# Performance work log

Measured on AMD Instinct MI355X. Metric: run time of the kernel, lower is better.

Reference implementation:

```python
import jax, jax.numpy as jnp
from jax import lax
import numpy as np

B, T, D, H = 256, 512, 64, 256

def setup_inputs() -> dict:
    key = jax.random.key(0)
    ks = jax.random.split(key, 15)
    s = lambda fan_in: 1.0 / np.sqrt(fan_in)
    def lin(k, out_d, in_d):
        k1, k2 = jax.random.split(k)
        return (jax.random.uniform(k1, (out_d, in_d), jnp.float32, -s(in_d), s(in_d)),
                jax.random.uniform(k2, (out_d,), jnp.float32, -s(in_d), s(in_d)))
    W1_w, W1_b = lin(ks[0], H, D)
    U1_w, U1_b = lin(ks[1], H, H)
    W2_w, W2_b = lin(ks[2], H, H)
    U2_w, U2_b = lin(ks[3], H, H)
    o1_w, o1_b = lin(ks[4], D, H)
    o2_w, o2_b = lin(ks[5], D, H)
    g_w, g_b = lin(ks[6], H, 2 * H)
    x = jax.random.normal(ks[7], (B, T, D), jnp.float32)
    return {"x": x, "W1_w": W1_w, "W1_b": W1_b, "U1_w": U1_w, "U1_b": U1_b,
            "W2_w": W2_w, "W2_b": W2_b, "U2_w": U2_w, "U2_b": U2_b,
            "o1_w": o1_w, "o1_b": o1_b, "o2_w": o2_w, "o2_b": o2_b,
            "g_w": g_w, "g_b": g_b}


def reference(x, W1_w, W1_b, U1_w, U1_b, W2_w, W2_b, U2_w, U2_b,
              o1_w, o1_b, o2_w, o2_b, g_w, g_b):
    Bb, Tt, Dd = x.shape
    Hh = U1_w.shape[0]
    h1_0 = jnp.zeros((Bb, Hh), x.dtype)
    h2_0 = jnp.zeros((Bb, Hh), x.dtype)
    u_0 = jnp.ones((Bb, Hh), x.dtype)  # initial gate = 1 (broadcast of ones(1,1))

    def step(carry, xt):
        h1, h2, u = carry
        h1 = jnp.tanh(xt @ W1_w.T + W1_b + h1 @ U1_w.T + U1_b)
        h2_new = jnp.tanh(h1 @ W2_w.T + W2_b + h2 @ U2_w.T + U2_b)
        h2 = u * h2_new + (1.0 - u) * h2
        out = h1 @ o1_w.T + o1_b + h2 @ o2_w.T + o2_b  # (B, D)
        u = jax.nn.sigmoid(jnp.concatenate([h1, h2], axis=1) @ g_w.T + g_b)
        return (h1, h2, u), out

    _, outs = lax.scan(step, (h1_0, h2_0, u_0), jnp.swapaxes(x, 0, 1))  # (T, B, D)
    return jnp.swapaxes(outs, 0, 1)  # (B, T, D)
```

## Files before the change

kernel.cpp:

```cpp
#include <hip/hip_runtime.h>

typedef unsigned short u16;
using bf8   = __attribute__((ext_vector_type(8))) short;
using bf4   = __attribute__((ext_vector_type(4))) short;
using f32x4 = __attribute__((ext_vector_type(4))) float;

#define B_ 256
#define T_ 512
#define D_ 64
#define H_ 256
#define Tc_ 64
#define NC_ (T_ / Tc_)
#define GEMMB_ 192

#define MFMA(a, b, c) __builtin_amdgcn_mfma_f32_16x16x32_bf16(a, b, c, 0, 0, 0)

static __device__ inline u16 f2b(float f) {
    unsigned int u = __float_as_uint(f);
    unsigned int r = (u + 0x7fffu + ((u >> 16) & 1u)) >> 16;
    return (u16)r;
}
static __device__ inline float fast_tanh(float x) {
    float e = __expf(2.f * x);
    return 1.f - 2.f / (e + 1.f);
}
static __device__ inline float fast_sigmoid(float x) {
    return 1.f / (1.f + __expf(-x));
}
static __device__ inline void lds_barrier() {
    asm volatile("s_waitcnt lgkmcnt(0)" ::: "memory");
    __builtin_amdgcn_s_barrier();
    asm volatile("" ::: "memory");
}

__global__ __launch_bounds__(256) void k_conv(
    const float* __restrict__ W1w, const float* __restrict__ U1w,
    const float* __restrict__ W2w, const float* __restrict__ U2w,
    const float* __restrict__ o1w, const float* __restrict__ o2w,
    const float* __restrict__ gw,
    u16* W1bf, u16* U1bf, u16* W2bf, u16* U2bf,
    u16* o1bf, u16* o2bf, u16* gbf)
{
    const int a = blockIdx.y;
    const float* src; u16* dst; int n;
    switch (a) {
        case 0: src = W1w; dst = W1bf; n = 16384;  break;
        case 1: src = U1w; dst = U1bf; n = 65536;  break;
        case 2: src = W2w; dst = W2bf; n = 65536;  break;
        case 3: src = U2w; dst = U2bf; n = 65536;  break;
        case 4: src = o1w; dst = o1bf; n = 16384;  break;
        case 5: src = o2w; dst = o2bf; n = 16384;  break;
        default: src = gw; dst = gbf;  n = 131072; break;
    }
    const int i = (blockIdx.x * 256 + threadIdx.x) * 4;
    if (i < n) {
        f32x4 v = *(const f32x4*)(src + i);
        bf4 o;
        o[0] = (short)f2b(v[0]); o[1] = (short)f2b(v[1]);
        o[2] = (short)f2b(v[2]); o[3] = (short)f2b(v[3]);
        *(bf4*)(dst + i) = o;
    }
}

__device__ void h1_role(
    const float* __restrict__ x, const u16* __restrict__ W1,
    const u16* __restrict__ U1, const float* __restrict__ W1b,
    const float* __restrict__ U1b, u16* __restrict__ H1,
    u16* __restrict__ h1state, int c, u16 (*buf)[16][H_ + 8])
{
    const int g = blockIdx.x;
    const int tid = threadIdx.x;
    const int w = tid >> 6, lane = tid & 63;
    const int col = lane & 15, quad = lane >> 4;
    const int t0 = c * Tc_;

    bf8 u1f[2][8], w1f[2][2];
    float bias[2];
#pragma unroll
    for (int i = 0; i < 2; ++i) {
        const int n = (w * 2 + i) * 16 + col;
#pragma unroll
        for (int kt = 0; kt < 8; ++kt)
            u1f[i][kt] = *(const bf8*)(U1 + (size_t)n * H_ + kt * 32 + quad * 8);
#pragma unroll
        for (int kt = 0; kt < 2; ++kt)
            w1f[i][kt] = *(const bf8*)(W1 + (size_t)n * D_ + kt * 32 + quad * 8);
        bias[i] = W1b[n] + U1b[n];
    }

    if (c == 0) {
        for (int idx = tid; idx < 16 * (H_ + 8); idx += 512)
            ((u16*)buf[0])[idx] = 0;
    } else {
        const int m = tid >> 5, hb = (tid & 31) * 8;
#pragma unroll
        for (int j = 0; j < 8; ++j)
            buf[0][m][hb + j] = h1state[(size_t)(g * 16 + m) * H_ + hb + j];
    }
    __syncthreads();

    const float* xrow = x + (size_t)(g * 16 + col) * T_ * D_ + quad * 8;
    f32x4 xa[4];
    {
        const float* xp = xrow + (size_t)t0 * D_;
        xa[0] = *(const f32x4*)xp;        xa[1] = *(const f32x4*)(xp + 4);
        xa[2] = *(const f32x4*)(xp + 32); xa[3] = *(const f32x4*)(xp + 36);
    }

    int p = 0;
    for (int tt = 0; tt < Tc_; ++tt) {
        const int tn = t0 + (tt + 1 < Tc_ ? tt + 1 : tt);
        f32x4 xan[4];
        {
            const float* xp = xrow + (size_t)tn * D_;
            xan[0] = *(const f32x4*)xp;        xan[1] = *(const f32x4*)(xp + 4);
            xan[2] = *(const f32x4*)(xp + 32); xan[3] = *(const f32x4*)(xp + 36);
        }
        bf8 haf[8];
#pragma unroll
        for (int kt = 0; kt < 8; ++kt)
            haf[kt] = *(const bf8*)&buf[p][col][kt * 32 + quad * 8];

        bf8 xaf[2];
#pragma unroll
        for (int kt = 0; kt < 2; ++kt) {
            bf8 v;
#pragma unroll
            for (int j = 0; j < 4; ++j) {
                v[j]     = (short)f2b(xa[kt * 2][j]);
                v[j + 4] = (short)f2b(xa[kt * 2 + 1][j]);
            }
            xaf[kt] = v;
        }

        f32x4 acc[2];
#pragma unroll
        for (int i = 0; i < 2; ++i) {
            acc[i][0] = bias[i]; acc[i][1] = bias[i];
            acc[i][2] = bias[i]; acc[i][3] = bias[i];
        }
#pragma unroll
        for (int kt = 0; kt < 8; ++kt)
#pragma unroll
            for (int i = 0; i < 2; ++i)
                acc[i] = MFMA(haf[kt], u1f[i][kt], acc[i]);
#pragma unroll
        for (int kt = 0; kt < 2; ++kt)
#pragma unroll
            for (int i = 0; i < 2; ++i)
                acc[i] = MFMA(xaf[kt], w1f[i][kt], acc[i]);

#pragma unroll
        for (int i = 0; i < 2; ++i) {
            const int n = (w * 2 + i) * 16 + col;
#pragma unroll
            for (int r = 0; r < 4; ++r)
                buf[p ^ 1][quad * 4 + r][n] = f2b(fast_tanh(acc[i][r]));
        }
        lds_barrier();
        {
            const int m = tid >> 5, hb = (tid & 31) * 8;
            bf8 v0 = *(const bf8*)&buf[p ^ 1][m][hb];
            *(bf8*)(H1 + ((size_t)tt * 256 + g * 16 + m) * H_ + hb) = v0;
        }
        xa[0] = xan[0]; xa[1] = xan[1]; xa[2] = xan[2]; xa[3] = xan[3];
        p ^= 1;
    }
    {
        const int m = tid >> 5, hb = (tid & 31) * 8;
#pragma unroll
        for (int j = 0; j < 8; ++j)
            h1state[(size_t)(g * 16 + m) * H_ + hb + j] = buf[p][m][hb + j];
    }
}

__device__ void h2_role(
    const u16* __restrict__ U2, const u16* __restrict__ gw,
    const float* __restrict__ W2c, const float* __restrict__ G1c,
    u16* __restrict__ H2, float* __restrict__ h2state,
    float* __restrict__ ustate, int ch, u16 (*buf)[16][H_ + 8])
{
    const int g = blockIdx.x - 16;
    const int tid = threadIdx.x;
    const int w = tid >> 6, lane = tid & 63;
    const int col = lane & 15, quad = lane >> 4;

    bf8 u2f[2][8], g2f[2][8];
#pragma unroll
    for (int i = 0; i < 2; ++i) {
        const int n = (w * 2 + i) * 16 + col;
#pragma unroll
        for (int kt = 0; kt < 8; ++kt) {
            u2f[i][kt] = *(const bf8*)(U2 + (size_t)n * H_ + kt * 32 + quad * 8);
            g2f[i][kt] = *(const bf8*)(gw + (size_t)n * (2 * H_) + H_ + kt * 32 + quad * 8);
        }
    }

    f32x4 h2p[2], up[2];
    if (ch == 0) {
#pragma unroll
        for (int i = 0; i < 2; ++i) {
            h2p[i][0]=0.f; h2p[i][1]=0.f; h2p[i][2]=0.f; h2p[i][3]=0.f;
            up[i][0]=1.f;  up[i][1]=1.f;  up[i][2]=1.f;  up[i][3]=1.f;
        }
    } else {
#pragma unroll
        for (int i = 0; i < 2; ++i) {
            size_t idx = (((size_t)g * 16 + (w * 2 + i)) * 64 + lane) * 4;
            h2p[i] = *(const f32x4*)(h2state + idx);
            up[i]  = *(const f32x4*)(ustate + idx);
        }
    }

#pragma unroll
    for (int i = 0; i < 2; ++i) {
        const int n = (w * 2 + i) * 16 + col;
#pragma unroll
        for (int r = 0; r < 4; ++r) buf[0][quad * 4 + r][n] = f2b(h2p[i][r]);
    }
    __syncthreads();
    bf8 h2af[8];
#pragma unroll
    for (int kt = 0; kt < 8; ++kt)
        h2af[kt] = *(const bf8*)&buf[0][col][kt * 32 + quad * 8];

    f32x4 w2cr[2];
#pragma unroll
    for (int i = 0; i < 2; ++i)
        w2cr[i] = *(const f32x4*)(W2c +
            ((((size_t)g * Tc_ + 0) * 16 + (w * 2 + i)) * 64 + lane) * 4);

    int p = 0;
    for (int tt = 0; tt < Tc_; ++tt) {
        const int ttn = (tt + 1 < Tc_) ? tt + 1 : tt;
        f32x4 w2cn[2], g1cc[2];
#pragma unroll
        for (int i = 0; i < 2; ++i) {
            w2cn[i] = *(const f32x4*)(W2c +
                ((((size_t)g * Tc_ + ttn) * 16 + (w * 2 + i)) * 64 + lane) * 4);
            g1cc[i] = *(const f32x4*)(G1c +
                ((((size_t)g * Tc_ + tt) * 16 + (w * 2 + i)) * 64 + lane) * 4);
        }

        f32x4 acc1[2];
#pragma unroll
        for (int i = 0; i < 2; ++i) acc1[i] = w2cr[i];
#pragma unroll
        for (int kt = 0; kt < 8; ++kt)
#pragma unroll
            for (int i = 0; i < 2; ++i)
                acc1[i] = MFMA(h2af[kt], u2f[i][kt], acc1[i]);

#pragma unroll
        for (int i = 0; i < 2; ++i)
#pragma unroll
            for (int r = 0; r < 4; ++r) {
                float h2n = fast_tanh(acc1[i][r]);
                h2p[i][r] = up[i][r] * h2n + (1.f - up[i][r]) * h2p[i][r];
            }
#pragma unroll
        for (int i = 0; i < 2; ++i) {
            const int n = (w * 2 + i) * 16 + col;
#pragma unroll
            for (int r = 0; r < 4; ++r) buf[p ^ 1][quad * 4 + r][n] = f2b(h2p[i][r]);
        }
        lds_barrier();
#pragma unroll
        for (int kt = 0; kt < 8; ++kt)
            h2af[kt] = *(const bf8*)&buf[p ^ 1][col][kt * 32 + quad * 8];
        {
            const int m = tid >> 5, hb = (tid & 31) * 8;
            bf8 v0 = *(const bf8*)&buf[p ^ 1][m][hb];
            *(bf8*)(H2 + ((size_t)tt * 256 + g * 16 + m) * H_ + hb) = v0;
        }

        f32x4 accg[2];
#pragma unroll
        for (int i = 0; i < 2; ++i) accg[i] = g1cc[i];
#pragma unroll
        for (int kt = 0; kt < 8; ++kt)
#pragma unroll
            for (int i = 0; i < 2; ++i)
                accg[i] = MFMA(h2af[kt], g2f[i][kt], accg[i]);
#pragma unroll
        for (int i = 0; i < 2; ++i)
#pragma unroll
            for (int r = 0; r < 4; ++r) up[i][r] = fast_sigmoid(accg[i][r]);

#pragma unroll
        for (int i = 0; i < 2; ++i) w2cr[i] = w2cn[i];
        p ^= 1;
    }
#pragma unroll
    for (int i = 0; i < 2; ++i) {
        size_t idx = (((size_t)g * 16 + (w * 2 + i)) * 64 + lane) * 4;
        *(f32x4*)(h2state + idx) = h2p[i];
        *(f32x4*)(ustate + idx)  = up[i];
    }
}

__global__ __launch_bounds__(512)
__attribute__((amdgpu_waves_per_eu(2, 2))) void k_pipe(
    const float* __restrict__ x, const u16* __restrict__ W1,
    const u16* __restrict__ U1, const float* __restrict__ W1b,
    const float* __restrict__ U1b, u16* __restrict__ H1w,
    u16* __restrict__ h1state,
    const u16* __restrict__ U2, const u16* __restrict__ gwgt,
    const float* __restrict__ W2cr, const float* __restrict__ G1cr,
    u16* __restrict__ H2w, float* __restrict__ h2state,
    float* __restrict__ ustate,
    const u16* __restrict__ H1r, const u16* __restrict__ W2,
    const u16* __restrict__ o1w, const u16* __restrict__ o2w,
    const float* __restrict__ W2b, const float* __restrict__ U2b,
    const float* __restrict__ gbias, const float* __restrict__ o1b,
    const float* __restrict__ o2b,
    float* __restrict__ W2cw, float* __restrict__ G1cw, float* __restrict__ O1cw,
    const u16* __restrict__ H2r, const float* __restrict__ O1r,
    float* __restrict__ out, int c)
{
    __shared__ __align__(16) u16 buf[2][16][H_ + 8];
    if (blockIdx.x < 16) {
        if (c < NC_)
            h1_role(x, W1, U1, W1b, U1b, H1w, h1state, c, buf);
    } else if (blockIdx.x < 32) {
        if (c >= 2 && c <= NC_ + 1)
            h2_role(U2, gwgt, W2cr, G1cr, H2w, h2state, ustate, c - 2, buf);
    } else {
        const int gbk = blockIdx.x - 32;
        const int tid = threadIdx.x;
        const int w = tid >> 6, lane = tid & 63;
        const int col = lane & 15, quad = lane >> 4;
        const int Wv = gbk * 8 + w;
        const int ny = Wv % 10;
        const int j  = Wv / 10;
        if (j >= 153) return;
        const bool act = (ny < 9) ? (c >= 1 && c <= NC_)
                                  : (c >= 3 && c <= NC_ + 2);
        if (!act) return;

        bf8 bfv[4][8];
        float bias[4];
#pragma unroll
        for (int i = 0; i < 4; ++i) {
            const int n = ny * 64 + i * 16 + col;
            const u16* bp; float bs;
            if (n < 256)      { bp = W2   + (size_t)n * H_;             bs = W2b[n] + U2b[n]; }
            else if (n < 512) { bp = gwgt + (size_t)(n - 256) * (2*H_); bs = gbias[n - 256]; }
            else if (n < 576) { bp = o1w  + (size_t)(n - 512) * H_;     bs = o1b[n-512] + o2b[n-512]; }
            else              { bp = o2w  + (size_t)(n - 576) * H_;     bs = 0.f; }
            bias[i] = bs;
#pragma unroll
            for (int kt = 0; kt < 8; ++kt)
                bfv[i][kt] = *(const bf8*)(bp + kt * 32 + quad * 8);
        }

        const u16* Ar = (ny < 9) ? H1r : H2r;
        float* Cb = W2cw; int ntb = 0;
        if (ny < 4)       { Cb = W2cw; ntb = ny * 4; }
        else if (ny < 8)  { Cb = G1cw; ntb = ny * 4 - 16; }
        else if (ny == 8) { Cb = O1cw; ntb = 0; }
        const int tb = (c - 3) * Tc_;

        for (int mt = j; mt < 1024; mt += 153) {
            const int mrow = mt * 16;
            f32x4 acc[4];
#pragma unroll
            for (int i = 0; i < 4; ++i) {
                acc[i][0] = bias[i]; acc[i][1] = bias[i];
                acc[i][2] = bias[i]; acc[i][3] = bias[i];
            }
#pragma unroll
            for (int kt = 0; kt < 8; ++kt) {
                bf8 af = *(const bf8*)(Ar + (size_t)(mrow + col) * H_ + kt * 32 + quad * 8);
#pragma unroll
                for (int i = 0; i < 4; ++i)
                    acc[i] = MFMA(af, bfv[i][kt], acc[i]);
            }
            const int tt = mrow >> 8, gg = (mrow & 255) >> 4;
            if (ny < 8) {
#pragma unroll
                for (int i = 0; i < 4; ++i) {
                    size_t idx = ((((size_t)gg * Tc_ + tt) * 16 + (ntb + i)) * 64 + lane) * 4;
                    *(f32x4*)(Cb + idx) = acc[i];
                }
            } else if (ny == 8) {
#pragma unroll
                for (int i = 0; i < 4; ++i) {
                    size_t idx = ((((size_t)gg * Tc_ + tt) * 4 + i) * 64 + lane) * 4;
                    *(f32x4*)(Cb + idx) = acc[i];
                }
            } else {
#pragma unroll
                for (int i = 0; i < 4; ++i) {
                    f32x4 o1v = *(const f32x4*)(O1r +
                        ((((size_t)gg * Tc_ + tt) * 4 + i) * 64 + lane) * 4);
#pragma unroll
                    for (int r = 0; r < 4; ++r)
                        out[((size_t)(gg * 16 + quad * 4 + r) * T_ + (tb + tt)) * D_ +
                            i * 16 + col] = acc[i][r] + o1v[r];
                }
            }
        }
    }
}

extern "C" void kernel_launch(void* const* d_in, const int* in_sizes, int n_in,
                              void* d_out, int out_size, void* d_ws, size_t ws_size,
                              hipStream_t stream)
{
    const float* x   = (const float*)d_in[0];
    const float* W1w = (const float*)d_in[1];
    const float* W1b = (const float*)d_in[2];
    const float* U1w = (const float*)d_in[3];
    const float* U1b = (const float*)d_in[4];
    const float* W2w = (const float*)d_in[5];
    const float* W2b = (const float*)d_in[6];
    const float* U2w = (const float*)d_in[7];
    const float* U2b = (const float*)d_in[8];
    const float* o1w = (const float*)d_in[9];
    const float* o1b = (const float*)d_in[10];
    const float* o2w = (const float*)d_in[11];
    const float* o2b = (const float*)d_in[12];
    const float* gw  = (const float*)d_in[13];
    const float* gb  = (const float*)d_in[14];
    float* out = (float*)d_out;
    (void)in_sizes; (void)n_in; (void)out_size; (void)ws_size;

    char* p = (char*)d_ws;
    u16* W1bf = (u16*)p; p += 16384 * 2;
    u16* U1bf = (u16*)p; p += 65536 * 2;
    u16* W2bf = (u16*)p; p += 65536 * 2;
    u16* U2bf = (u16*)p; p += 65536 * 2;
    u16* o1bf = (u16*)p; p += 16384 * 2;
    u16* o2bf = (u16*)p; p += 16384 * 2;
    u16* gbf  = (u16*)p; p += 131072 * 2;
    u16* H1[2]; u16* H2[2]; float* W2c[2]; float* G1c[2]; float* O1c[3];
    for (int pa = 0; pa < 2; ++pa) {
        H1[pa]  = (u16*)p;   p += (size_t)Tc_ * 131072;
        H2[pa]  = (u16*)p;   p += (size_t)Tc_ * 131072;
        W2c[pa] = (float*)p; p += (size_t)Tc_ * 262144;
        G1c[pa] = (float*)p; p += (size_t)Tc_ * 262144;
    }
    for (int pa = 0; pa < 3; ++pa) {
        O1c[pa] = (float*)p; p += (size_t)Tc_ * 65536;
    }
    u16* h1s   = (u16*)p;  p += 131072;
    float* h2s = (float*)p; p += 262144;
    float* us  = (float*)p;

    k_conv<<<dim3(128, 7), 256, 0, stream>>>(W1w, U1w, W2w, U2w, o1w, o2w, gw,
                                             W1bf, U1bf, W2bf, U2bf, o1bf, o2bf, gbf);

    for (int c = 0; c <= NC_ + 2; ++c) {
        const int pw  = c & 1;
        const int pg  = (c + 1) & 1;
        const int ph  = c & 1;
        const int s_w = ((c - 1) % 3 + 3) % 3;
        const int s_r = ((c - 3) % 3 + 3) % 3;
        k_pipe<<<32 + GEMMB_, 512, 0, stream>>>(
            x, W1bf, U1bf, W1b, U1b, H1[pw], h1s,
            U2bf, gbf, W2c[ph], G1c[ph], H2[pw], h2s, us,
            H1[pg], W2bf, o1bf, o2bf, W2b, U2b, gb, o1b, o2b,
            W2c[pg], G1c[pg], O1c[s_w],
            H2[pg], O1c[s_r], out, c);
    }
}
```

Measured before the change: 1.204 ms.

## Double block size to 1024 threads, one 16-column tile per wave

After: 1.604 ms. 1.33x slower.

```diff
diff --git a/kernel.cpp b/kernel.cpp
--- a/kernel.cpp
+++ b/kernel.cpp
@@ -11,7 +11,7 @@
 #define H_ 256
 #define Tc_ 64
 #define NC_ (T_ / Tc_)
-#define GEMMB_ 192
+#define GEMMB_ 190
 
 #define MFMA(a, b, c) __builtin_amdgcn_mfma_f32_16x16x32_bf16(a, b, c, 0, 0, 0)
 
@@ -73,29 +73,24 @@
     const int w = tid >> 6, lane = tid & 63;
     const int col = lane & 15, quad = lane >> 4;
     const int t0 = c * Tc_;
-
-    bf8 u1f[2][8], w1f[2][2];
-    float bias[2];
-#pragma unroll
-    for (int i = 0; i < 2; ++i) {
-        const int n = (w * 2 + i) * 16 + col;
-#pragma unroll
-        for (int kt = 0; kt < 8; ++kt)
-            u1f[i][kt] = *(const bf8*)(U1 + (size_t)n * H_ + kt * 32 + quad * 8);
-#pragma unroll
-        for (int kt = 0; kt < 2; ++kt)
-            w1f[i][kt] = *(const bf8*)(W1 + (size_t)n * D_ + kt * 32 + quad * 8);
-        bias[i] = W1b[n] + U1b[n];
-    }
+    const int n = w * 16 + col;
+
+    bf8 u1f[8], w1f[2];
+#pragma unroll
+    for (int kt = 0; kt < 8; ++kt)
+        u1f[kt] = *(const bf8*)(U1 + (size_t)n * H_ + kt * 32 + quad * 8);
+#pragma unroll
+    for (int kt = 0; kt < 2; ++kt)
+        w1f[kt] = *(const bf8*)(W1 + (size_t)n * D_ + kt * 32 + quad * 8);
+    const float bias = W1b[n] + U1b[n];
 
     if (c == 0) {
-        for (int idx = tid; idx < 16 * (H_ + 8); idx += 512)
+        for (int idx = tid; idx < 16 * (H_ + 8); idx += 1024)
             ((u16*)buf[0])[idx] = 0;
     } else {
-        const int m = tid >> 5, hb = (tid & 31) * 8;
-#pragma unroll
-        for (int j = 0; j < 8; ++j)
-            buf[0][m][hb + j] = h1state[(size_t)(g * 16 + m) * H_ + hb + j];
+        const int m = tid >> 6, hb = (tid & 63) * 4;
+        *(bf4*)&buf[0][m][hb] =
+            *(const bf4*)(h1state + (size_t)(g * 16 + m) * H_ + hb);
     }
     __syncthreads();
 
@@ -133,44 +128,31 @@
             xaf[kt] = v;
         }
 
-        f32x4 acc[2];
-#pragma unroll
-        for (int i = 0; i < 2; ++i) {
-            acc[i][0] = bias[i]; acc[i][1] = bias[i];
-            acc[i][2] = bias[i]; acc[i][3] = bias[i];
-        }
+        f32x4 acc;
+        acc[0] = bias; acc[1] = bias; acc[2] = bias; acc[3] = bias;
 #pragma unroll
         for (int kt = 0; kt < 8; ++kt)
-#pragma unroll
-            for (int i = 0; i < 2; ++i)
-                acc[i] = MFMA(haf[kt], u1f[i][kt], acc[i]);
+            acc = MFMA(haf[kt], u1f[kt], acc);
 #pragma unroll
         for (int kt = 0; kt < 2; ++kt)
-#pragma unroll
-            for (int i = 0; i < 2; ++i)
-                acc[i] = MFMA(xaf[kt], w1f[i][kt], acc[i]);
-
-#pragma unroll
-        for (int i = 0; i < 2; ++i) {
-            const int n = (w * 2 + i) * 16 + col;
-#pragma unroll
-            for (int r = 0; r < 4; ++r)
-                buf[p ^ 1][quad * 4 + r][n] = f2b(fast_tanh(acc[i][r]));
-        }
+            acc = MFMA(xaf[kt], w1f[kt], acc);
+
+#pragma unroll
+        for (int r = 0; r < 4; ++r)
+            buf[p ^ 1][quad * 4 + r][n] = f2b(fast_tanh(acc[r]));
         lds_barrier();
         {
-            const int m = tid >> 5, hb = (tid & 31) * 8;
-            bf8 v0 = *(const bf8*)&buf[p ^ 1][m][hb];
-            *(bf8*)(H1 + ((size_t)tt * 256 + g * 16 + m) * H_ + hb) = v0;
+            const int m = tid >> 6, hb = (tid & 63) * 4;
+            bf4 v0 = *(const bf4*)&buf[p ^ 1][m][hb];
+            *(bf4*)(H1 + ((size_t)tt * 256 + g * 16 + m) * H_ + hb) = v0;
         }
         xa[0] = xan[0]; xa[1] = xan[1]; xa[2] = xan[2]; xa[3] = xan[3];
         p ^= 1;
     }
     {
-        const int m = tid >> 5, hb = (tid & 31) * 8;
-#pragma unroll
-        for (int j = 0; j < 8; ++j)
-            h1state[(size_t)(g * 16 + m) * H_ + hb + j] = buf[p][m][hb + j];
+        const int m = tid >> 6, hb = (tid & 63) * 4;
+        *(bf4*)(h1state + (size_t)(g * 16 + m) * H_ + hb) =
+            *(const bf4*)&buf[p][m][hb];
     }
 }
 
@@ -184,123 +166,84 @@
     const int tid = threadIdx.x;
     const int w = tid >> 6, lane = tid & 63;
     const int col = lane & 15, quad = lane >> 4;
-
-    bf8 u2f[2][8], g2f[2][8];
-#pragma unroll
-    for (int i = 0; i < 2; ++i) {
-        const int n = (w * 2 + i) * 16 + col;
-#pragma unroll
-        for (int kt = 0; kt < 8; ++kt) {
-            u2f[i][kt] = *(const bf8*)(U2 + (size_t)n * H_ + kt * 32 + quad * 8);
-            g2f[i][kt] = *(const bf8*)(gw + (size_t)n * (2 * H_) + H_ + kt * 32 + quad * 8);
-        }
-    }
-
-    f32x4 h2p[2], up[2];
+    const int n = w * 16 + col;
+
+    bf8 u2f[8], g2f[8];
+#pragma unroll
+    for (int kt = 0; kt < 8; ++kt) {
+        u2f[kt] = *(const bf8*)(U2 + (size_t)n * H_ + kt * 32 + quad * 8);
+        g2f[kt] = *(const bf8*)(gw + (size_t)n * (2 * H_) + H_ + kt * 32 + quad * 8);
+    }
+
+    f32x4 h2p, up;
     if (ch == 0) {
-#pragma unroll
-        for (int i = 0; i < 2; ++i) {
-            h2p[i][0]=0.f; h2p[i][1]=0.f; h2p[i][2]=0.f; h2p[i][3]=0.f;
-            up[i][0]=1.f;  up[i][1]=1.f;  up[i][2]=1.f;  up[i][3]=1.f;
-        }
+        h2p[0]=0.f; h2p[1]=0.f; h2p[2]=0.f; h2p[3]=0.f;
+        up[0]=1.f;  up[1]=1.f;  up[2]=1.f;  up[3]=1.f;
     } else {
-#pragma unroll
-        for (int i = 0; i < 2; ++i) {
-            size_t idx = (((size_t)g * 16 + (w * 2 + i)) * 64 + lane) * 4;
-            h2p[i] = *(const f32x4*)(h2state + idx);
-            up[i]  = *(const f32x4*)(ustate + idx);
-        }
-    }
-
-#pragma unroll
-    for (int i = 0; i < 2; ++i) {
-        const int n = (w * 2 + i) * 16 + col;
-#pragma unroll
-        for (int r = 0; r < 4; ++r) buf[0][quad * 4 + r][n] = f2b(h2p[i][r]);
-    }
+        size_t idx = (((size_t)g * 16 + w) * 64 + lane) * 4;
+        h2p = *(const f32x4*)(h2state + idx);
+        up  = *(const f32x4*)(ustate + idx);
+    }
+
+#pragma unroll
+    for (int r = 0; r < 4; ++r) buf[0][quad * 4 + r][n] = f2b(h2p[r]);
     __syncthreads();
     bf8 h2af[8];
 #pragma unroll
     for (int kt = 0; kt < 8; ++kt)
         h2af[kt] = *(const bf8*)&buf[0][col][kt * 32 + quad * 8];
 
-    f32x4 w2cr[2];
-#pragma unroll
-    for (int i = 0; i < 2; ++i)
-        w2cr[i] = *(const f32x4*)(W2c +
-            ((((size_t)g * Tc_ + 0) * 16 + (w * 2 + i)) * 64 + lane) * 4);
+    f32x4 w2cr = *(const f32x4*)(W2c +
+        ((((size_t)g * Tc_ + 0) * 16 + w) * 64 + lane) * 4);
 
     int p = 0;
     for (int tt = 0; tt < Tc_; ++tt) {
         const int ttn = (tt + 1 < Tc_) ? tt + 1 : tt;
-        f32x4 w2cn[2], g1cc[2];
-#pragma unroll
-        for (int i = 0; i < 2; ++i) {
-            w2cn[i] = *(const f32x4*)(W2c +
-                ((((size_t)g * Tc_ + ttn) * 16 + (w * 2 + i)) * 64 + lane) * 4);
-            g1cc[i] = *(const f32x4*)(G1c +
-                ((((size_t)g * Tc_ + tt) * 16 + (w * 2 + i)) * 64 + lane) * 4);
-        }
-
-        f32x4 acc1[2];
-#pragma unroll
-        for (int i = 0; i < 2; ++i) acc1[i] = w2cr[i];
+        f32x4 w2cn = *(const f32x4*)(W2c +
+            ((((size_t)g * Tc_ + ttn) * 16 + w) * 64 + lane) * 4);
+        f32x4 g1cc = *(const f32x4*)(G1c +
+            ((((size_t)g * Tc_ + tt) * 16 + w) * 64 + lane) * 4);
+
+        f32x4 acc1 = w2cr;
 #pragma unroll
         for (int kt = 0; kt < 8; ++kt)
-#pragma unroll
-            for (int i = 0; i < 2; ++i)
-                acc1[i] = MFMA(h2af[kt], u2f[i][kt], acc1[i]);
-
-#pragma unroll
-        for (int i = 0; i < 2; ++i)
-#pragma unroll
-            for (int r = 0; r < 4; ++r) {
-                float h2n = fast_tanh(acc1[i][r]);
-                h2p[i][r] = up[i][r] * h2n + (1.f - up[i][r]) * h2p[i][r];
-            }
-#pragma unroll
-        for (int i = 0; i < 2; ++i) {
-            const int n = (w * 2 + i) * 16 + col;
-#pragma unroll
-            for (int r = 0; r < 4; ++r) buf[p ^ 1][quad * 4 + r][n] = f2b(h2p[i][r]);
-        }
+            acc1 = MFMA(h2af[kt], u2f[kt], acc1);
+
+#pragma unroll
+        for (int r = 0; r < 4; ++r) {
+            float h2n = fast_tanh(acc1[r]);
+            h2p[r] = up[r] * h2n + (1.f - up[r]) * h2p[r];
+        }
+#pragma unroll
+        for (int r = 0; r < 4; ++r) buf[p ^ 1][quad * 4 + r][n] = f2b(h2p[r]);
         lds_barrier();
 #pragma unroll
         for (int kt = 0; kt < 8; ++kt)
             h2af[kt] = *(const bf8*)&buf[p ^ 1][col][kt * 32 + quad * 8];
         {
-            const int m = tid >> 5, hb = (tid & 31) * 8;
-            bf8 v0 = *(const bf8*)&buf[p ^ 1][m][hb];
-            *(bf8*)(H2 + ((size_t)tt * 256 + g * 16 + m) * H_ + hb) = v0;
-        }
-
-        f32x4 accg[2];
-#pragma unroll
-        for (int i = 0; i < 2; ++i) accg[i] = g1cc[i];
+            const int m = tid >> 6, hb = (tid & 63) * 4;
+            bf4 v0 = *(const bf4*)&buf[p ^ 1][m][hb];
+            *(bf4*)(H2 + ((size_t)tt * 256 + g * 16 + m) * H_ + hb) = v0;
+        }
+
+        f32x4 accg = g1cc;
 #pragma unroll
         for (int kt = 0; kt < 8; ++kt)
-#pragma unroll
-            for (int i = 0; i < 2; ++i)
-                accg[i] = MFMA(h2af[kt], g2f[i][kt], accg[i]);
-#pragma unroll
-        for (int i = 0; i < 2; ++i)
-#pragma unroll
-            for (int r = 0; r < 4; ++r) up[i][r] = fast_sigmoid(accg[i][r]);
-
-#pragma unroll
-        for (int i = 0; i < 2; ++i) w2cr[i] = w2cn[i];
+            accg = MFMA(h2af[kt], g2f[kt], accg);
+#pragma unroll
+        for (int r = 0; r < 4; ++r) up[r] = fast_sigmoid(accg[r]);
+
+        w2cr = w2cn;
         p ^= 1;
     }
-#pragma unroll
-    for (int i = 0; i < 2; ++i) {
-        size_t idx = (((size_t)g * 16 + (w * 2 + i)) * 64 + lane) * 4;
-        *(f32x4*)(h2state + idx) = h2p[i];
-        *(f32x4*)(ustate + idx)  = up[i];
-    }
-}
-
-__global__ __launch_bounds__(512)
-__attribute__((amdgpu_waves_per_eu(2, 2))) void k_pipe(
+    {
+        size_t idx = (((size_t)g * 16 + w) * 64 + lane) * 4;
+        *(f32x4*)(h2state + idx) = h2p;
+        *(f32x4*)(ustate + idx)  = up;
+    }
+}
+
+__global__ __launch_bounds__(1024) void k_pipe(
     const float* __restrict__ x, const u16* __restrict__ W1,
     const u16* __restrict__ U1, const float* __restrict__ W1b,
     const float* __restrict__ U1b, u16* __restrict__ H1w,
@@ -330,74 +273,77 @@
         const int tid = threadIdx.x;
         const int w = tid >> 6, lane = tid & 63;
         const int col = lane & 15, quad = lane >> 4;
-        const int Wv = gbk * 8 + w;
-        const int ny = Wv % 10;
-        const int j  = Wv / 10;
-        if (j >= 153) return;
-        const bool act = (ny < 9) ? (c >= 1 && c <= NC_)
-                                  : (c >= 3 && c <= NC_ + 2);
+        const int Wv = gbk * 16 + w;
+        const int unit = Wv % 20;
+        const int j = Wv / 20;
+        const bool act = (unit < 18) ? (c >= 1 && c <= NC_)
+                                     : (c >= 3 && c <= NC_ + 2);
         if (!act) return;
 
-        bf8 bfv[4][8];
-        float bias[4];
-#pragma unroll
-        for (int i = 0; i < 4; ++i) {
-            const int n = ny * 64 + i * 16 + col;
+        bf8 bfv[2][8];
+        float bias[2];
+#pragma unroll
+        for (int i = 0; i < 2; ++i) {
             const u16* bp; float bs;
-            if (n < 256)      { bp = W2   + (size_t)n * H_;             bs = W2b[n] + U2b[n]; }
-            else if (n < 512) { bp = gwgt + (size_t)(n - 256) * (2*H_); bs = gbias[n - 256]; }
-            else if (n < 576) { bp = o1w  + (size_t)(n - 512) * H_;     bs = o1b[n-512] + o2b[n-512]; }
-            else              { bp = o2w  + (size_t)(n - 576) * H_;     bs = 0.f; }
+            if (unit < 18) {
+                const int n = unit * 32 + i * 16 + col;
+                if (n < 256)      { bp = W2   + (size_t)n * H_;             bs = W2b[n] + U2b[n]; }
+                else if (n < 512) { bp = gwgt + (size_t)(n - 256) * (2*H_); bs = gbias[n - 256]; }
+                else              { bp = o1w  + (size_t)(n - 512) * H_;     bs = o1b[n-512] + o2b[n-512]; }
+            } else {
+                const int n = (unit - 18) * 32 + i * 16 + col;
+                bp = o2w + (size_t)n * H_; bs = 0.f;
+            }
             bias[i] = bs;
 #pragma unroll
             for (int kt = 0; kt < 8; ++kt)
                 bfv[i][kt] = *(const bf8*)(bp + kt * 32 + quad * 8);
         }
 
-        const u16* Ar = (ny < 9) ? H1r : H2r;
-        float* Cb = W2cw; int ntb = 0;
-        if (ny < 4)       { Cb = W2cw; ntb = ny * 4; }
-        else if (ny < 8)  { Cb = G1cw; ntb = ny * 4 - 16; }
-        else if (ny == 8) { Cb = O1cw; ntb = 0; }
+        const u16* Ar = (unit < 18) ? H1r : H2r;
         const int tb = (c - 3) * Tc_;
 
-        for (int mt = j; mt < 1024; mt += 153) {
+        for (int mt = j; mt < 1024; mt += 152) {
             const int mrow = mt * 16;
-            f32x4 acc[4];
-#pragma unroll
-            for (int i = 0; i < 4; ++i) {
+            f32x4 acc[2];
+#pragma unroll
+            for (int i = 0; i < 2; ++i) {
                 acc[i][0] = bias[i]; acc[i][1] = bias[i];
                 acc[i][2] = bias[i]; acc[i][3] = bias[i];
             }
 #pragma unroll
             for (int kt = 0; kt < 8; ++kt) {
                 bf8 af = *(const bf8*)(Ar + (size_t)(mrow + col) * H_ + kt * 32 + quad * 8);
-#pragma unroll
-                for (int i = 0; i < 4; ++i)
-                    acc[i] = MFMA(af, bfv[i][kt], acc[i]);
+                acc[0] = MFMA(af, bfv[0][kt], acc[0]);
+                acc[1] = MFMA(af, bfv[1][kt], acc[1]);
             }
-            const int tt = mrow >> 8, gg = (mrow & 255) >> 4;
-            if (ny < 8) {
-#pragma unroll
-                for (int i = 0; i < 4; ++i) {
-                    size_t idx = ((((size_t)gg * Tc_ + tt) * 16 + (ntb + i)) * 64 + lane) * 4;
+            const int tt = mt >> 4, gg = mt & 15;
+            if (unit < 16) {
+#pragma unroll
+                for (int i = 0; i < 2; ++i) {
+                    const int nt = unit * 2 + i;
+                    float* Cb = (nt < 16) ? W2cw : G1cw;
+                    const int nn = nt & 15;
+                    size_t idx = ((((size_t)gg * Tc_ + tt) * 16 + nn) * 64 + lane) * 4;
                     *(f32x4*)(Cb + idx) = acc[i];
                 }
-            } else if (ny == 8) {
-#pragma unroll
-                for (int i = 0; i < 4; ++i) {
-                    size_t idx = ((((size_t)gg * Tc_ + tt) * 4 + i) * 64 + lane) * 4;
-                    *(f32x4*)(Cb + idx) = acc[i];
+            } else if (unit < 18) {
+#pragma unroll
+                for (int i = 0; i < 2; ++i) {
+                    const int ot = (unit - 16) * 2 + i;
+                    size_t idx = ((((size_t)gg * Tc_ + tt) * 4 + ot) * 64 + lane) * 4;
+                    *(f32x4*)(O1cw + idx) = acc[i];
                 }
             } else {
 #pragma unroll
-                for (int i = 0; i < 4; ++i) {
+                for (int i = 0; i < 2; ++i) {
+                    const int ot = (unit - 18) * 2 + i;
                     f32x4 o1v = *(const f32x4*)(O1r +
-                        ((((size_t)gg * Tc_ + tt) * 4 + i) * 64 + lane) * 4);
+                        ((((size_t)gg * Tc_ + tt) * 4 + ot) * 64 + lane) * 4);
 #pragma unroll
                     for (int r = 0; r < 4; ++r)
                         out[((size_t)(gg * 16 + quad * 4 + r) * T_ + (tb + tt)) * D_ +
-                            i * 16 + col] = acc[i][r] + o1v[r];
+                            ot * 16 + col] = acc[i][r] + o1v[r];
                 }
             }
         }
@@ -457,7 +403,7 @@
         const int ph  = c & 1;
         const int s_w = ((c - 1) % 3 + 3) % 3;
         const int s_r = ((c - 3) % 3 + 3) % 3;
-        k_pipe<<<32 + GEMMB_, 512, 0, stream>>>(
+        k_pipe<<<32 + GEMMB_, 1024, 0, stream>>>(
             x, W1bf, U1bf, W1b, U1b, H1[pw], h1s,
             U2bf, gbf, W2c[ph], G1c[ph], H2[pw], h2s, us,
             H1[pg], W2bf, o1bf, o2bf, W2b, U2b, gb, o1b, o2b,
```

## Stage recurrent U1/U2 weights in LDS instead of registers

Applied to the files above, without the earlier changes.

New measurement: 1.359 ms. +12.9%, slower.

```diff
diff --git a/kernel.cpp b/kernel.cpp
--- a/kernel.cpp
+++ b/kernel.cpp
@@ -31,6 +31,15 @@
     asm volatile("s_waitcnt lgkmcnt(0)" ::: "memory");
     __builtin_amdgcn_s_barrier();
     asm volatile("" ::: "memory");
+}
+
+static __device__ inline void stage_weights(
+    u16* __restrict__ wlds, const u16* __restrict__ W, int tid)
+{
+    for (int idx = tid; idx < 8192; idx += 512) {
+        const int n = idx & 255, kc = idx >> 8;
+        *(bf8*)&wlds[(size_t)idx * 8] = *(const bf8*)(W + (size_t)n * 256 + kc * 8);
+    }
 }
 
 __global__ __launch_bounds__(256) void k_conv(
@@ -66,22 +75,24 @@
     const float* __restrict__ x, const u16* __restrict__ W1,
     const u16* __restrict__ U1, const float* __restrict__ W1b,
     const float* __restrict__ U1b, u16* __restrict__ H1,
-    u16* __restrict__ h1state, int c, u16 (*buf)[16][H_ + 8])
+    u16* __restrict__ h1state, int c, u16 (*buf)[16][H_ + 8],
+    u16* __restrict__ wlds)
 {
     const int g = blockIdx.x;
     const int tid = threadIdx.x;
     const int w = tid >> 6, lane = tid & 63;
     const int col = lane & 15, quad = lane >> 4;
     const int t0 = c * Tc_;
-
-    bf8 u1f[2][8], w1f[2][2];
+    const int n0 = (w * 2) * 16 + col;
+    const int n1 = (w * 2 + 1) * 16 + col;
+
+    stage_weights(wlds, U1, tid);
+
+    bf8 w1f[2][2];
     float bias[2];
 #pragma unroll
     for (int i = 0; i < 2; ++i) {
         const int n = (w * 2 + i) * 16 + col;
-#pragma unroll
-        for (int kt = 0; kt < 8; ++kt)
-            u1f[i][kt] = *(const bf8*)(U1 + (size_t)n * H_ + kt * 32 + quad * 8);
 #pragma unroll
         for (int kt = 0; kt < 2; ++kt)
             w1f[i][kt] = *(const bf8*)(W1 + (size_t)n * D_ + kt * 32 + quad * 8);
@@ -116,10 +127,21 @@
             xan[0] = *(const f32x4*)xp;        xan[1] = *(const f32x4*)(xp + 4);
             xan[2] = *(const f32x4*)(xp + 32); xan[3] = *(const f32x4*)(xp + 36);
         }
-        bf8 haf[8];
-#pragma unroll
-        for (int kt = 0; kt < 8; ++kt)
-            haf[kt] = *(const bf8*)&buf[p][col][kt * 32 + quad * 8];
+
+        f32x4 acc[2];
+#pragma unroll
+        for (int i = 0; i < 2; ++i) {
+            acc[i][0] = bias[i]; acc[i][1] = bias[i];
+            acc[i][2] = bias[i]; acc[i][3] = bias[i];
+        }
+#pragma unroll
+        for (int kt = 0; kt < 8; ++kt) {
+            bf8 hf = *(const bf8*)&buf[p][col][kt * 32 + quad * 8];
+            bf8 u0 = *(const bf8*)&wlds[(size_t)(((kt * 4 + quad) * 256) + n0) * 8];
+            bf8 u1v = *(const bf8*)&wlds[(size_t)(((kt * 4 + quad) * 256) + n1) * 8];
+            acc[0] = MFMA(hf, u0, acc[0]);
+            acc[1] = MFMA(hf, u1v, acc[1]);
+        }
 
         bf8 xaf[2];
 #pragma unroll
@@ -132,18 +154,6 @@
             }
             xaf[kt] = v;
         }
-
-        f32x4 acc[2];
-#pragma unroll
-        for (int i = 0; i < 2; ++i) {
-            acc[i][0] = bias[i]; acc[i][1] = bias[i];
-            acc[i][2] = bias[i]; acc[i][3] = bias[i];
-        }
-#pragma unroll
-        for (int kt = 0; kt < 8; ++kt)
-#pragma unroll
-            for (int i = 0; i < 2; ++i)
-                acc[i] = MFMA(haf[kt], u1f[i][kt], acc[i]);
 #pragma unroll
         for (int kt = 0; kt < 2; ++kt)
 #pragma unroll
@@ -178,22 +188,25 @@
     const u16* __restrict__ U2, const u16* __restrict__ gw,
     const float* __restrict__ W2c, const float* __restrict__ G1c,
     u16* __restrict__ H2, float* __restrict__ h2state,
-    float* __restrict__ ustate, int ch, u16 (*buf)[16][H_ + 8])
+    float* __restrict__ ustate, int ch, u16 (*buf)[16][H_ + 8],
+    u16* __restrict__ wlds)
 {
     const int g = blockIdx.x - 16;
     const int tid = threadIdx.x;
     const int w = tid >> 6, lane = tid & 63;
     const int col = lane & 15, quad = lane >> 4;
-
-    bf8 u2f[2][8], g2f[2][8];
+    const int n0 = (w * 2) * 16 + col;
+    const int n1 = (w * 2 + 1) * 16 + col;
+
+    stage_weights(wlds, U2, tid);
+
+    bf8 g2f[2][8];
 #pragma unroll
     for (int i = 0; i < 2; ++i) {
         const int n = (w * 2 + i) * 16 + col;
 #pragma unroll
-        for (int kt = 0; kt < 8; ++kt) {
-            u2f[i][kt] = *(const bf8*)(U2 + (size_t)n * H_ + kt * 32 + quad * 8);
+        for (int kt = 0; kt < 8; ++kt)
             g2f[i][kt] = *(const bf8*)(gw + (size_t)n * (2 * H_) + H_ + kt * 32 + quad * 8);
-        }
     }
 
     f32x4 h2p[2], up[2];
@@ -219,43 +232,37 @@
         for (int r = 0; r < 4; ++r) buf[0][quad * 4 + r][n] = f2b(h2p[i][r]);
     }
     __syncthreads();
-    bf8 h2af[8];
-#pragma unroll
-    for (int kt = 0; kt < 8; ++kt)
-        h2af[kt] = *(const bf8*)&buf[0][col][kt * 32 + quad * 8];
-
-    f32x4 w2cr[2];
-#pragma unroll
-    for (int i = 0; i < 2; ++i)
-        w2cr[i] = *(const f32x4*)(W2c +
-            ((((size_t)g * Tc_ + 0) * 16 + (w * 2 + i)) * 64 + lane) * 4);
 
     int p = 0;
     for (int tt = 0; tt < Tc_; ++tt) {
-        const int ttn = (tt + 1 < Tc_) ? tt + 1 : tt;
-        f32x4 w2cn[2], g1cc[2];
-#pragma unroll
-        for (int i = 0; i < 2; ++i) {
-            w2cn[i] = *(const f32x4*)(W2c +
-                ((((size_t)g * Tc_ + ttn) * 16 + (w * 2 + i)) * 64 + lane) * 4);
+        f32x4 w2cc[2], g1cc[2];
+#pragma unroll
+        for (int i = 0; i < 2; ++i) {
+            w2cc[i] = *(const f32x4*)(W2c +
+                ((((size_t)g * Tc_ + tt) * 16 + (w * 2 + i)) * 64 + lane) * 4);
             g1cc[i] = *(const f32x4*)(G1c +
                 ((((size_t)g * Tc_ + tt) * 16 + (w * 2 + i)) * 64 + lane) * 4);
         }
 
         f32x4 acc1[2];
 #pragma unroll
-        for (int i = 0; i < 2; ++i) acc1[i] = w2cr[i];
-#pragma unroll
-        for (int kt = 0; kt < 8; ++kt)
-#pragma unroll
-            for (int i = 0; i < 2; ++i)
-                acc1[i] = MFMA(h2af[kt], u2f[i][kt], acc1[i]);
+        for (int i = 0; i < 2; ++i) {
+            acc1[i][0]=0.f; acc1[i][1]=0.f; acc1[i][2]=0.f; acc1[i][3]=0.f;
+        }
+#pragma unroll
+        for (int kt = 0; kt < 8; ++kt) {
+            bf8 hf = *(const bf8*)&buf[p][col][kt * 32 + quad * 8];
+            bf8 u0 = *(const bf8*)&wlds[(size_t)(((kt * 4 + quad) * 256) + n0) * 8];
+            bf8 u1v = *(const bf8*)&wlds[(size_t)(((kt * 4 + quad) * 256) + n1) * 8];
+            acc1[0] = MFMA(hf, u0, acc1[0]);
+            acc1[1] = MFMA(hf, u1v, acc1[1]);
+        }
 
 #pragma unroll
         for (int i = 0; i < 2; ++i)
 #pragma unroll
             for (int r = 0; r < 4; ++r) {
-                float h2n = fast_tanh(acc1[i][r]);
+                float h2n = fast_tanh(acc1[i][r] + w2cc[i][r]);
                 h2p[i][r] = up[i][r] * h2n + (1.f - up[i][r]) * h2p[i][r];
             }
 #pragma unroll
@@ -265,9 +272,6 @@
             for (int r = 0; r < 4; ++r) buf[p ^ 1][quad * 4 + r][n] = f2b(h2p[i][r]);
         }
         lds_barrier();
-#pragma unroll
-        for (int kt = 0; kt < 8; ++kt)
-            h2af[kt] = *(const bf8*)&buf[p ^ 1][col][kt * 32 + quad * 8];
         {
             const int m = tid >> 5, hb = (tid & 31) * 8;
             bf8 v0 = *(const bf8*)&buf[p ^ 1][m][hb];
@@ -278,17 +282,16 @@
 #pragma unroll
         for (int i = 0; i < 2; ++i) accg[i] = g1cc[i];
 #pragma unroll
-        for (int kt = 0; kt < 8; ++kt)
-#pragma unroll
-            for (int i = 0; i < 2; ++i)
-                accg[i] = MFMA(h2af[kt], g2f[i][kt], accg[i]);
+        for (int kt = 0; kt < 8; ++kt) {
+            bf8 hf = *(const bf8*)&buf[p ^ 1][col][kt * 32 + quad * 8];
+            accg[0] = MFMA(hf, g2f[0][kt], accg[0]);
+            accg[1] = MFMA(hf, g2f[1][kt], accg[1]);
+        }
 #pragma unroll
         for (int i = 0; i < 2; ++i)
 #pragma unroll
             for (int r = 0; r < 4; ++r) up[i][r] = fast_sigmoid(accg[i][r]);
 
-#pragma unroll
-        for (int i = 0; i < 2; ++i) w2cr[i] = w2cn[i];
         p ^= 1;
     }
 #pragma unroll
@@ -299,8 +302,7 @@
     }
 }
 
-__global__ __launch_bounds__(512)
-__attribute__((amdgpu_waves_per_eu(2, 2))) void k_pipe(
+__global__ __launch_bounds__(512) void k_pipe(
     const float* __restrict__ x, const u16* __restrict__ W1,
     const u16* __restrict__ U1, const float* __restrict__ W1b,
     const float* __restrict__ U1b, u16* __restrict__ H1w,
@@ -319,12 +321,13 @@
     float* __restrict__ out, int c)
 {
     __shared__ __align__(16) u16 buf[2][16][H_ + 8];
+    __shared__ __align__(16) u16 wlds[65536];
     if (blockIdx.x < 16) {
         if (c < NC_)
-            h1_role(x, W1, U1, W1b, U1b, H1w, h1state, c, buf);
+            h1_role(x, W1, U1, W1b, U1b, H1w, h1state, c, buf, wlds);
     } else if (blockIdx.x < 32) {
         if (c >= 2 && c <= NC_ + 1)
-            h2_role(U2, gwgt, W2cr, G1cr, H2w, h2state, ustate, c - 2, buf);
+            h2_role(U2, gwgt, W2cr, G1cr, H2w, h2state, ustate, c - 2, buf, wlds);
     } else {
         const int gbk = blockIdx.x - 32;
         const int tid = threadIdx.x;
@@ -387,7 +390,7 @@
 #pragma unroll
                 for (int i = 0; i < 4; ++i) {
                     size_t idx = ((((size_t)gg * Tc_ + tt) * 4 + i) * 64 + lane) * 4;
-                    *(f32x4*)(Cb + idx) = acc[i];
+                    *(f32x4*)(O1cw + idx) = acc[i];
                 }
             } else {
 #pragma unroll
```
